# Kernel tuning notes

Measured on AMD Instinct MI355X. Metric: run time of the kernel, lower is better.

The kernel has to match this reference:

```python
import jax, jax.numpy as jnp
import numpy as np

B, S, H, STEPS = 4096, 169, 64, 24  # batch, input seq (window 168 + covariate row), hidden, rollout steps


def _lstm(xseq, Wih, Whh, bih, bhh, h0, c0):
    """PyTorch-style single-layer LSTM. xseq: [B,T,D] -> ([B,T,H], hT, cT). Gate order i,f,g,o."""
    xg = jnp.einsum('btd,gd->btg', xseq, Wih) + (bih + bhh)  # precompute input proj [B,T,4H]

    def step(carry, xg_t):
        h, c = carry
        g = xg_t + h @ Whh.T
        i, f, gg, o = jnp.split(g, 4, axis=-1)
        c = jax.nn.sigmoid(f) * c + jax.nn.sigmoid(i) * jnp.tanh(gg)
        h = jax.nn.sigmoid(o) * jnp.tanh(c)
        return (h, c), h

    (hT, cT), hs = jax.lax.scan(step, (h0, c0), jnp.swapaxes(xg, 0, 1))
    return jnp.swapaxes(hs, 0, 1), hT, cT


def reference(x, Wih1, Whh1, bih1, bhh1, Wih2, Whh2, bih2, bhh2, fc1_w, fc1_b, fc2_w, fc2_b):
    win, d = x[:, :-1, :], x[:, -1, :]  # [B,168,1], [B,1]
    z = jnp.zeros((x.shape[0], H), x.dtype)

    def outer(win, _):
        h1s, h1, c1 = _lstm(win, Wih1, Whh1, bih1, bhh1, z, z)
        h1s = jax.nn.relu(h1s)
        # lstm2 is seeded with lstm1's final (h, c) state, as in the torch code
        h2s, _, _ = _lstm(h1s, Wih2, Whh2, bih2, bhh2, h1, c1)
        feat = jnp.concatenate([jax.nn.relu(h2s[:, -1, :]), d], axis=1)  # [B,65]
        out = (feat @ fc1_w.T + fc1_b) @ fc2_w.T + fc2_b  # [B,1] (no relu between fc1/fc2)
        win = jnp.concatenate([win[:, 1:, :], out[:, :, None]], axis=1)  # slide window
        return win, out[:, 0]

    _, outs = jax.lax.scan(outer, win, None, length=STEPS)  # outs: [24,B]
    return jnp.swapaxes(outs, 0, 1)  # [B,24]


def setup_inputs() -> dict:
    key = jax.random.key(0)
    ks = jax.random.split(key, 14)
    bnd = 1.0 / np.sqrt(H)

    def u(k, shape):
        return jax.random.uniform(k, shape, jnp.float32, -bnd, bnd)

    return {
        'x': jax.random.normal(ks[0], (B, S, 1), jnp.float32),
        'Wih1': u(ks[1], (4 * H, 1)),
        'Whh1': u(ks[2], (4 * H, H)),
        'bih1': u(ks[3], (4 * H,)),
        'bhh1': u(ks[4], (4 * H,)),
        'Wih2': u(ks[5], (4 * H, H)),
        'Whh2': u(ks[6], (4 * H, H)),
        'bih2': u(ks[7], (4 * H,)),
        'bhh2': u(ks[8], (4 * H,)),
        'fc1_w': u(ks[9], (64, 65)),
        'fc1_b': u(ks[10], (64,)),
        'fc2_w': u(ks[11], (1, 64)),
        'fc2_b': u(ks[12], (1,)),
    }
```

## Files before the change

kernel.cpp:

```cpp
#include <hip/hip_runtime.h>
#include <stdint.h>

#define NB 16
#define WIN 168
#define NSTEPS 24
#define NBLK (4096/NB)
#define NT 512

typedef __attribute__((ext_vector_type(8))) short bf16x8;
typedef __attribute__((ext_vector_type(4))) float f32x4;

#if __has_builtin(__builtin_amdgcn_rcpf)
#define RCPF(x) __builtin_amdgcn_rcpf(x)
#else
#define RCPF(x) (1.0f / (x))
#endif
#if __has_builtin(__builtin_amdgcn_exp2f)
#define EXP2F(x) __builtin_amdgcn_exp2f(x)
#else
#define EXP2F(x) __expf((x) * 0.6931471805599453f)
#endif

__device__ __forceinline__ float sigm(float x){
  return RCPF(1.0f + EXP2F(x * -1.4426950408889634f));
}
__device__ __forceinline__ float sigtanh(float a, float b){
  float A = EXP2F(a * -1.4426950408889634f);
  float B = EXP2F(fabsf(b) * -2.8853900817779268f);
  float t = (1.0f - B) * RCPF((1.0f + A) * (1.0f + B));
  uint32_t sb = __builtin_bit_cast(uint32_t, b) & 0x80000000u;
  return __builtin_bit_cast(float, __builtin_bit_cast(uint32_t, t) ^ sb);
}

__device__ __forceinline__ uint32_t bf_rn(float f){
  uint32_t u = __builtin_bit_cast(uint32_t, f);
  return (u + 0x7FFFu + ((u >> 16) & 1u)) >> 16;
}
__device__ __forceinline__ float bf_f(uint32_t s){
  return __builtin_bit_cast(float, s << 16);
}
__device__ __forceinline__ void split_t(float f, uint32_t& hi, uint32_t& lo){
  uint32_t u = __builtin_bit_cast(uint32_t, f);
  hi = u >> 16;
  lo = bf_rn(f - bf_f(hi));
}
__device__ __forceinline__ void split_s(float f, short& hi, short& lo){
  uint32_t h = bf_rn(f);
  hi = (short)h;
  lo = (short)bf_rn(f - bf_f(h));
}
__device__ __forceinline__ f32x4 mfma16(bf16x8 a, bf16x8 b, f32x4 c){
  return __builtin_amdgcn_mfma_f32_16x16x32_bf16(a, b, c, 0, 0, 0);
}

__device__ __forceinline__ void lstm_epi(const f32x4 acc[4], float c[4], float hn[4]){
  #pragma unroll
  for (int r = 0; r < 4; r++){
    float cn = __builtin_fmaf(sigm(acc[1][r]), c[r], sigtanh(acc[0][r], acc[2][r]));
    c[r] = cn;
    hn[r] = sigtanh(acc[3][r], cn);
  }
}

#define FROW 136
#define FBLK 544
#define FB(buf,hl,kt) ((((buf)*2 + (hl))*2 + (kt)) * FBLK)
#define BUF_INTS (2*FBLK)

__global__ __launch_bounds__(NT, 2) void lstm_fused_kernel(
  const float* __restrict__ x,    const float* __restrict__ Wih1, const float* __restrict__ Whh1,
  const float* __restrict__ bih1, const float* __restrict__ bhh1,
  const float* __restrict__ Wih2, const float* __restrict__ Whh2,
  const float* __restrict__ bih2, const float* __restrict__ bhh2,
  const float* __restrict__ fc1w, const float* __restrict__ fc1b,
  const float* __restrict__ fc2w, const float* __restrict__ fc2b,
  float* __restrict__ out, short* __restrict__ hist)
{
  __shared__ __align__(16) short aS[2*2*2*FBLK];
  __shared__ __align__(16) short bS[2*2*2*FBLK];
  __shared__ float cS[64][16];
  __shared__ float win_s[WIN][NB];
  __shared__ float Hlast[NB][68];
  __shared__ float fc1w_s[64*68];
  __shared__ float dval_s[NB];

  const int tid = threadIdx.x;
  const int wv8 = tid >> 6;
  const int wv  = wv8 & 3;
  const bool isA = (wv8 < 4);
  const int ln  = tid & 63;
  const int q   = ln >> 4;
  const int n   = ln & 15;
  const int bg0 = blockIdx.x * NB;
  const int u0  = 16*wv + 4*q;
  const int kt_  = u0 >> 5;
  const int q2_  = (u0 >> 3) & 3;
  const int jj0_ = u0 & 7;
  const int rdo  = q*FROW + n*8;
  const int wro  = q2_*FROW + n*8 + jj0_;
  const int gwo  = kt_*512 + q2_*128 + n*8 + jj0_;
  const int ro   = q*128 + n*8;
  short* __restrict__ hblk = hist + (size_t)blockIdx.x * WIN * 2048;

  for (int i = tid; i < WIN*NB; i += NT){ int t = i >> 4, b = i & 15; win_s[t][b] = x[(bg0 + b)*169 + t]; }
  for (int i = tid; i < 64*65; i += NT){ int j = i / 65, k = i % 65; fc1w_s[j*68 + k] = fc1w[i]; }
  if (tid < NB) dval_s[tid] = x[(bg0 + tid)*169 + 168];

  const float fc1b_r = fc1b[ln];
  const float fc2w_r = fc2w[ln];
  const float fc2b_r = fc2b[0];

  auto fc_head = [&](int s){
    float o2[2];
    #pragma unroll
    for (int bi = 0; bi < 2; bi++){
      const int b = 2*wv8 + bi;
      float a1 = fc1b_r;
      #pragma unroll
      for (int k4 = 0; k4 < 16; k4++){
        const float* wp = &fc1w_s[ln*68 + k4*4];
        const float* hp = &Hlast[b][k4*4];
        a1 += wp[0]*hp[0] + wp[1]*hp[1] + wp[2]*hp[2] + wp[3]*hp[3];
      }
      a1 += dval_s[b] * fc1w_s[ln*68 + 64];
      float v = a1 * fc2w_r;
      #pragma unroll
      for (int off = 32; off > 0; off >>= 1) v += __shfl_xor(v, off);
      o2[bi] = v + fc2b_r;
    }
    if (ln == 0){
      #pragma unroll
      for (int bi = 0; bi < 2; bi++){
        const int b = 2*wv8 + bi;
        out[(bg0 + b)*24 + s] = o2[bi];
        win_s[s % WIN][b] = o2[bi];
      }
    }
  };

  if (isA){
    bf16x8 A1hi[4][2], A1lo[4][2], Ain1[4];
    f32x4 b1c[4];
    #pragma unroll
    for (int e = 0; e < 4; e++){
      const int ja = 64*e + 16*wv + n;
      #pragma unroll
      for (int kt = 0; kt < 2; kt++){
        const float* p = Whh1 + ja*64 + kt*32 + q*8;
        #pragma unroll
        for (int jj = 0; jj < 8; jj++){ short h,l; split_s(p[jj], h, l); A1hi[e][kt][jj] = h; A1lo[e][kt][jj] = l; }
      }
      bf16x8 ain = {0,0,0,0,0,0,0,0};
      if (q == 0){ short wh, wl; split_s(Wih1[ja], wh, wl); ain[0] = wh; ain[1] = wh; ain[2] = wl; }
      Ain1[e] = ain;
      const int jc = 64*e + u0;
      #pragma unroll
      for (int r = 0; r < 4; r++) b1c[e][r] = bih1[jc+r] + bhh1[jc+r];
    }
    float c1[4];

    auto lstm1 = [&](int rb, int wb, int slot, int t, bool first){
      f32x4 acc[4];
      bf16x8 bin = {0,0,0,0,0,0,0,0};
      { float xv = win_s[slot][n]; uint32_t xh, xl; split_t(xv, xh, xl);
        if (q == 0){ bin[0] = (short)xh; bin[1] = (short)xl; bin[2] = (short)xh; } }
      if (first){
        #pragma unroll
        for (int e = 0; e < 4; e++) acc[e] = mfma16(Ain1[e], bin, b1c[e]);
      } else {
        bf16x8 Bh0 = *(const bf16x8*)&aS[FB(rb,0,0)+rdo];
        bf16x8 Bl0 = *(const bf16x8*)&aS[FB(rb,1,0)+rdo];
        bf16x8 Bh1 = *(const bf16x8*)&aS[FB(rb,0,1)+rdo];
        bf16x8 Bl1 = *(const bf16x8*)&aS[FB(rb,1,1)+rdo];
        #pragma unroll
        for (int e = 0; e < 4; e++){
          f32x4 a = b1c[e];
          a = mfma16(A1hi[e][0], Bh0, a);
          a = mfma16(A1hi[e][0], Bl0, a);
          a = mfma16(A1lo[e][0], Bh0, a);
          a = mfma16(A1hi[e][1], Bh1, a);
          a = mfma16(A1hi[e][1], Bl1, a);
          a = mfma16(A1lo[e][1], Bh1, a);
          a = mfma16(Ain1[e], bin, a);
          acc[e] = a;
        }
      }
      float hn[4];
      lstm_epi(acc, c1, hn);
      uint32_t ph[4], pl[4];
      #pragma unroll
      for (int r = 0; r < 4; r++) split_t(hn[r], ph[r], pl[r]);
      *(uint2*)&aS[FB(wb,0,kt_)+wro] = make_uint2(ph[0] | (ph[1]<<16), ph[2] | (ph[3]<<16));
      *(uint2*)&aS[FB(wb,1,kt_)+wro] = make_uint2(pl[0] | (pl[1]<<16), pl[2] | (pl[3]<<16));
      uint32_t sh[4], sl[4];
      #pragma unroll
      for (int r = 0; r < 4; r++){ bool pos = hn[r] > 0.0f; sh[r] = pos ? ph[r] : 0u; sl[r] = pos ? pl[r] : 0u; }
      short* Hp = hblk + (size_t)t * 2048;
      *(uint2*)&Hp[gwo]        = make_uint2(sh[0] | (sh[1]<<16), sh[2] | (sh[3]<<16));
      *(uint2*)&Hp[1024 + gwo] = make_uint2(sl[0] | (sl[1]<<16), sl[2] | (sl[3]<<16));
    };

    #pragma unroll
    for (int r = 0; r < 4; r++) c1[r] = 0.0f;
    for (int t = 0; t < WIN; t++){
      __syncthreads();
      lstm1(t & 1, (t & 1) ^ 1, t, t, t == 0);
    }
    #pragma unroll
    for (int r = 0; r < 4; r++) cS[u0 + r][n] = c1[r];

    for (int sg = 1; sg < NSTEPS; sg++){
      #pragma unroll
      for (int r = 0; r < 4; r++) c1[r] = 0.0f;
      int slot = sg;
      __syncthreads();
      lstm1(0, 1, slot, 0, true);
      slot++;
      for (int t = 1; t < WIN-1; t++){
        __syncthreads();
        lstm1(t & 1, (t & 1) ^ 1, slot, t, false);
        slot++; if (slot == WIN) slot = 0;
      }
      __syncthreads();
      __syncthreads();
      fc_head(sg - 1);
      __syncthreads();
      lstm1(1, 0, slot, WIN-1, false);
      #pragma unroll
      for (int r = 0; r < 4; r++) cS[u0 + r][n] = c1[r];
    }

    for (int i = 0; i < WIN + 1; i++) __syncthreads();
    fc_head(NSTEPS - 1);

  } else {
    bf16x8 A2hi[4][4], A2lo[4][4];
    f32x4 b2c[4];
    #pragma unroll
    for (int e = 0; e < 4; e++){
      const int ja = 64*e + 16*wv + n;
      #pragma unroll
      for (int kt = 0; kt < 4; kt++){
        const float* p = (kt < 2 ? (Wih2 + ja*64 + kt*32) : (Whh2 + ja*64 + (kt-2)*32)) + q*8;
        #pragma unroll
        for (int jj = 0; jj < 8; jj++){ short h,l; split_s(p[jj], h, l); A2hi[e][kt][jj] = h; A2lo[e][kt][jj] = l; }
      }
      const int jc = 64*e + u0;
      #pragma unroll
      for (int r = 0; r < 4; r++) b2c[e][r] = bih2[jc+r] + bhh2[jc+r];
    }
    float c2[4];
    bf16x8 ch0, cl0, ch1, cl1, nh0, nl0, nh1, nl1;

    auto loadc = [&](int t){
      const short* Hp = hblk + (size_t)t * 2048;
      ch0 = *(const bf16x8*)&Hp[ro];
      cl0 = *(const bf16x8*)&Hp[1024 + ro];
      ch1 = *(const bf16x8*)&Hp[512 + ro];
      cl1 = *(const bf16x8*)&Hp[1536 + ro];
    };
    auto loadn = [&](int t){
      const short* Hp = hblk + (size_t)t * 2048;
      nh0 = *(const bf16x8*)&Hp[ro];
      nl0 = *(const bf16x8*)&Hp[1024 + ro];
      nh1 = *(const bf16x8*)&Hp[512 + ro];
      nl1 = *(const bf16x8*)&Hp[1536 + ro];
    };
    auto shift = [&](){ ch0 = nh0; cl0 = nl0; ch1 = nh1; cl1 = nl1; };

    auto lstm2 = [&](const short* Sr, int rb, short* Sw, int wb, bool last){
      bf16x8 L2h0 = *(const bf16x8*)&Sr[FB(rb,0,0)+rdo];
      bf16x8 L2l0 = *(const bf16x8*)&Sr[FB(rb,1,0)+rdo];
      bf16x8 L2h1 = *(const bf16x8*)&Sr[FB(rb,0,1)+rdo];
      bf16x8 L2l1 = *(const bf16x8*)&Sr[FB(rb,1,1)+rdo];
      f32x4 acc[4];
      #pragma unroll
      for (int e = 0; e < 4; e++){
        f32x4 a = b2c[e];
        a = mfma16(A2hi[e][0], ch0, a);
        a = mfma16(A2hi[e][0], cl0, a);
        a = mfma16(A2lo[e][0], ch0, a);
        a = mfma16(A2hi[e][1], ch1, a);
        a = mfma16(A2hi[e][1], cl1, a);
        a = mfma16(A2lo[e][1], ch1, a);
        a = mfma16(A2hi[e][2], L2h0, a);
        a = mfma16(A2hi[e][2], L2l0, a);
        a = mfma16(A2lo[e][2], L2h0, a);
        a = mfma16(A2hi[e][3], L2h1, a);
        a = mfma16(A2hi[e][3], L2l1, a);
        a = mfma16(A2lo[e][3], L2h1, a);
        acc[e] = a;
      }
      float hn[4];
      lstm_epi(acc, c2, hn);
      if (!last){
        uint32_t ph[4], pl[4];
        #pragma unroll
        for (int r = 0; r < 4; r++) split_t(hn[r], ph[r], pl[r]);
        *(uint2*)&Sw[FB(wb,0,kt_)+wro] = make_uint2(ph[0] | (ph[1]<<16), ph[2] | (ph[3]<<16));
        *(uint2*)&Sw[FB(wb,1,kt_)+wro] = make_uint2(pl[0] | (pl[1]<<16), pl[2] | (pl[3]<<16));
      } else {
        #pragma unroll
        for (int r = 0; r < 4; r++) Hlast[n][u0 + r] = fmaxf(hn[r], 0.0f);
      }
    };

    for (int i = 0; i < WIN; i++) __syncthreads();

    for (int sg = 1; sg < NSTEPS; sg++){
      loadc(0);
      loadn(1);
      __syncthreads();
      #pragma unroll
      for (int r = 0; r < 4; r++) c2[r] = cS[u0 + r][n];
      lstm2(aS, 0, bS, 1, false);
      shift();
      for (int t = 1; t < WIN-1; t++){
        loadn(t + 1);
        __syncthreads();
        lstm2(bS, t & 1, bS, (t & 1) ^ 1, false);
        shift();
      }
      __syncthreads();
      lstm2(bS, 1, bS, 0, true);
      __syncthreads();
      fc_head(sg - 1);
      __syncthreads();
    }

    {
      loadc(0);
      loadn(1);
      __syncthreads();
      #pragma unroll
      for (int r = 0; r < 4; r++) c2[r] = cS[u0 + r][n];
      lstm2(aS, 0, bS, 1, false);
      shift();
      for (int t = 1; t < WIN; t++){
        if (t < WIN-1) loadn(t + 1);
        __syncthreads();
        lstm2(bS, t & 1, bS, (t & 1) ^ 1, t == WIN-1);
        shift();
      }
      __syncthreads();
      fc_head(NSTEPS - 1);
    }
  }
}

__global__ __launch_bounds__(256, 1) void lstm_fallback_kernel(
  const float* __restrict__ x,    const float* __restrict__ Wih1, const float* __restrict__ Whh1,
  const float* __restrict__ bih1, const float* __restrict__ bhh1,
  const float* __restrict__ Wih2, const float* __restrict__ Whh2,
  const float* __restrict__ bih2, const float* __restrict__ bhh2,
  const float* __restrict__ fc1w, const float* __restrict__ fc1b,
  const float* __restrict__ fc2w, const float* __restrict__ fc2b,
  float* __restrict__ out)
{
  __shared__ __align__(16) short aS[2*2*2*FBLK];
  __shared__ __align__(16) short r1f[2*2*2*FBLK];
  __shared__ __align__(16) short rlf[2*2*2*FBLK];
  __shared__ float win_s[WIN][NB];
  __shared__ float Hlast[NB][68];
  __shared__ float fc1w_s[64*68];
  __shared__ float dval_s[NB];

  const int tid = threadIdx.x;
  const int wv  = tid >> 6;
  const int ln  = tid & 63;
  const int q   = ln >> 4;
  const int n   = ln & 15;
  const int bg0 = blockIdx.x * NB;
  const int u0  = 16*wv + 4*q;
  const int kt_  = u0 >> 5;
  const int q2_  = (u0 >> 3) & 3;
  const int jj0_ = u0 & 7;
  const int rdo  = q*FROW + n*8;
  const int wro  = q2_*FROW + n*8 + jj0_;

  for (int i = tid; i < WIN*NB; i += 256){ int t = i >> 4, b = i & 15; win_s[t][b] = x[(bg0 + b)*169 + t]; }
  for (int i = tid; i < 64*65; i += 256){ int j = i / 65, k = i % 65; fc1w_s[j*68 + k] = fc1w[i]; }
  if (tid < NB) dval_s[tid] = x[(bg0 + tid)*169 + 168];

  const float fc1b_r = fc1b[ln];
  const float fc2w_r = fc2w[ln];
  const float fc2b_r = fc2b[0];

  bf16x8 A1hi[4][2], A1lo[4][2], Ain1[4];
  bf16x8 A2hi[4][4], A2lo[4][4];
  f32x4 b1c[4], b2c[4];
  #pragma unroll
  for (int e = 0; e < 4; e++){
    const int ja = 64*e + 16*wv + n;
    #pragma unroll
    for (int kt = 0; kt < 2; kt++){
      const float* p = Whh1 + ja*64 + kt*32 + q*8;
      #pragma unroll
      for (int jj = 0; jj < 8; jj++){ short h,l; split_s(p[jj], h, l); A1hi[e][kt][jj] = h; A1lo[e][kt][jj] = l; }
    }
    #pragma unroll
    for (int kt = 0; kt < 4; kt++){
      const float* p = (kt < 2 ? (Wih2 + ja*64 + kt*32) : (Whh2 + ja*64 + (kt-2)*32)) + q*8;
      #pragma unroll
      for (int jj = 0; jj < 8; jj++){ short h,l; split_s(p[jj], h, l); A2hi[e][kt][jj] = h; A2lo[e][kt][jj] = l; }
    }
    bf16x8 ain = {0,0,0,0,0,0,0,0};
    if (q == 0){ short wh, wl; split_s(Wih1[ja], wh, wl); ain[0] = wh; ain[1] = wh; ain[2] = wl; }
    Ain1[e] = ain;
    const int jc = 64*e + u0;
    #pragma unroll
    for (int r = 0; r < 4; r++){
      b1c[e][r] = bih1[jc+r] + bhh1[jc+r];
      b2c[e][r] = bih2[jc+r] + bhh2[jc+r];
    }
  }

  float c1[4], c2[4], c1r[4];

  auto lstm1_step = [&](short* S, float* cst, int rb, int wb, int slot, bool relu_out){
    bf16x8 Bh0 = *(const bf16x8*)&S[FB(rb,0,0)+rdo];
    bf16x8 Bl0 = *(const bf16x8*)&S[FB(rb,1,0)+rdo];
    bf16x8 Bh1 = *(const bf16x8*)&S[FB(rb,0,1)+rdo];
    bf16x8 Bl1 = *(const bf16x8*)&S[FB(rb,1,1)+rdo];
    bf16x8 bin = {0,0,0,0,0,0,0,0};
    { float xv = win_s[slot][n]; uint32_t xh, xl; split_t(xv, xh, xl);
      if (q == 0){ bin[0] = (short)xh; bin[1] = (short)xl; bin[2] = (short)xh; } }
    f32x4 acc[4];
    #pragma unroll
    for (int e = 0; e < 4; e++){
      f32x4 a = b1c[e];
      a = mfma16(A1hi[e][0], Bh0, a);
      a = mfma16(A1hi[e][0], Bl0, a);
      a = mfma16(A1lo[e][0], Bh0, a);
      a = mfma16(A1hi[e][1], Bh1, a);
      a = mfma16(A1hi[e][1], Bl1, a);
      a = mfma16(A1lo[e][1], Bh1, a);
      a = mfma16(Ain1[e], bin, a);
      acc[e] = a;
    }
    float hn[4];
    lstm_epi(acc, cst, hn);
    uint32_t ph[4], pl[4];
    #pragma unroll
    for (int r = 0; r < 4; r++) split_t(hn[r], ph[r], pl[r]);
    *(uint2*)&S[FB(wb,0,kt_)+wro] = make_uint2(ph[0] | (ph[1]<<16), ph[2] | (ph[3]<<16));
    *(uint2*)&S[FB(wb,1,kt_)+wro] = make_uint2(pl[0] | (pl[1]<<16), pl[2] | (pl[3]<<16));
    if (relu_out){
      uint32_t sh[4], sl[4];
      #pragma unroll
      for (int r = 0; r < 4; r++){ bool pos = hn[r] > 0.0f; sh[r] = pos ? ph[r] : 0u; sl[r] = pos ? pl[r] : 0u; }
      *(uint2*)&rlf[FB(rb,0,kt_)+wro] = make_uint2(sh[0] | (sh[1]<<16), sh[2] | (sh[3]<<16));
      *(uint2*)&rlf[FB(rb,1,kt_)+wro] = make_uint2(sl[0] | (sl[1]<<16), sl[2] | (sl[3]<<16));
    }
  };

  auto lstm2_core = [&](bf16x8 L1h0, bf16x8 L1l0, bf16x8 L1h1, bf16x8 L1l1,
                        int rbuf, int wbuf, bool last){
    bf16x8 L2h0 = *(const bf16x8*)&aS[FB(rbuf,0,0)+rdo];
    bf16x8 L2l0 = *(const bf16x8*)&aS[FB(rbuf,1,0)+rdo];
    bf16x8 L2h1 = *(const bf16x8*)&aS[FB(rbuf,0,1)+rdo];
    bf16x8 L2l1 = *(const bf16x8*)&aS[FB(rbuf,1,1)+rdo];
    f32x4 acc[4];
    #pragma unroll
    for (int e = 0; e < 4; e++){
      f32x4 a = b2c[e];
      a = mfma16(A2hi[e][0], L1h0, a);
      a = mfma16(A2hi[e][0], L1l0, a);
      a = mfma16(A2lo[e][0], L1h0, a);
      a = mfma16(A2hi[e][1], L1h1, a);
      a = mfma16(A2hi[e][1], L1l1, a);
      a = mfma16(A2lo[e][1], L1h1, a);
      a = mfma16(A2hi[e][2], L2h0, a);
      a = mfma16(A2hi[e][2], L2l0, a);
      a = mfma16(A2lo[e][2], L2h0, a);
      a = mfma16(A2hi[e][3], L2h1, a);
      a = mfma16(A2hi[e][3], L2l1, a);
      a = mfma16(A2lo[e][3], L2h1, a);
      acc[e] = a;
    }
    float hn[4];
    lstm_epi(acc, c2, hn);
    if (!last){
      uint32_t ph[4], pl[4];
      #pragma unroll
      for (int r = 0; r < 4; r++) split_t(hn[r], ph[r], pl[r]);
      *(uint2*)&aS[FB(wbuf,0,kt_)+wro] = make_uint2(ph[0] | (ph[1]<<16), ph[2] | (ph[3]<<16));
      *(uint2*)&aS[FB(wbuf,1,kt_)+wro] = make_uint2(pl[0] | (pl[1]<<16), pl[2] | (pl[3]<<16));
    } else {
      #pragma unroll
      for (int r = 0; r < 4; r++) Hlast[n][u0 + r] = fmaxf(hn[r], 0.0f);
    }
  };

  for (int s = 0; s < NSTEPS; s++){
    { int* p = (int*)&aS[0];
      for (int i = tid; i < BUF_INTS; i += 256) p[i] = 0; }
    #pragma unroll
    for (int r = 0; r < 4; r++) c1[r] = 0.0f;
    int slot = s;
    for (int t = 0; t < WIN; t++){
      __syncthreads();
      lstm1_step(aS, c1, t & 1, (t & 1) ^ 1, slot, false);
      slot++; if (slot == WIN) slot = 0;
    }
    #pragma unroll
    for (int r = 0; r < 4; r++){ c2[r] = c1[r]; c1r[r] = 0.0f; }
    { int* p = (int*)&r1f[0];
      for (int i = tid; i < BUF_INTS; i += 256) p[i] = 0; }
    slot = s;
    __syncthreads();
    lstm1_step(r1f, c1r, 0, 1, slot, true);
    slot++;
    for (int i = 1; i < WIN; i++){
      __syncthreads();
      const int rb = i & 1, wb = rb ^ 1;
      lstm1_step(r1f, c1r, rb, wb, slot, true);
      bf16x8 L1h0 = *(const bf16x8*)&rlf[FB(wb,0,0)+rdo];
      bf16x8 L1l0 = *(const bf16x8*)&rlf[FB(wb,1,0)+rdo];
      bf16x8 L1h1 = *(const bf16x8*)&rlf[FB(wb,0,1)+rdo];
      bf16x8 L1l1 = *(const bf16x8*)&rlf[FB(wb,1,1)+rdo];
      lstm2_core(L1h0, L1l0, L1h1, L1l1, wb, rb, false);
      slot++; if (slot == WIN) slot = 0;
    }
    __syncthreads();
    {
      const int rb = (WIN - 1) & 1;
      bf16x8 L1h0 = *(const bf16x8*)&rlf[FB(rb,0,0)+rdo];
      bf16x8 L1l0 = *(const bf16x8*)&rlf[FB(rb,1,0)+rdo];
      bf16x8 L1h1 = *(const bf16x8*)&rlf[FB(rb,0,1)+rdo];
      bf16x8 L1l1 = *(const bf16x8*)&rlf[FB(rb,1,1)+rdo];
      lstm2_core(L1h0, L1l0, L1h1, L1l1, rb, 0, true);
    }
    __syncthreads();
    {
      float o4[4];
      #pragma unroll
      for (int bi = 0; bi < 4; bi++){
        const int b = 4*wv + bi;
        float a1 = fc1b_r;
        #pragma unroll
        for (int k4 = 0; k4 < 16; k4++){
          const float* wp = &fc1w_s[ln*68 + k4*4];
          const float* hp = &Hlast[b][k4*4];
          a1 += wp[0]*hp[0] + wp[1]*hp[1] + wp[2]*hp[2] + wp[3]*hp[3];
        }
        a1 += dval_s[b] * fc1w_s[ln*68 + 64];
        float v = a1 * fc2w_r;
        #pragma unroll
        for (int off = 32; off > 0; off >>= 1) v += __shfl_xor(v, off);
        o4[bi] = v + fc2b_r;
      }
      if (ln == 0){
        #pragma unroll
        for (int bi = 0; bi < 4; bi++){
          const int b = 4*wv + bi;
          out[(bg0 + b)*24 + s] = o4[bi];
          win_s[s % WIN][b] = o4[bi];
        }
      }
    }
  }
}

extern "C" void kernel_launch(void* const* d_in, const int* in_sizes, int n_in,
                              void* d_out, int out_size, void* d_ws, size_t ws_size,
                              hipStream_t stream) {
  (void)in_sizes; (void)n_in; (void)out_size;
  const size_t need = (size_t)NBLK * WIN * 2048 * sizeof(short);
  if (ws_size >= need){
    lstm_fused_kernel<<<dim3(NBLK), dim3(NT), 0, stream>>>(
        (const float*)d_in[0], (const float*)d_in[1], (const float*)d_in[2],
        (const float*)d_in[3], (const float*)d_in[4], (const float*)d_in[5],
        (const float*)d_in[6], (const float*)d_in[7], (const float*)d_in[8],
        (const float*)d_in[9], (const float*)d_in[10], (const float*)d_in[11],
        (const float*)d_in[12], (float*)d_out, (short*)d_ws);
  } else {
    lstm_fallback_kernel<<<dim3(NBLK), dim3(256), 0, stream>>>(
        (const float*)d_in[0], (const float*)d_in[1], (const float*)d_in[2],
        (const float*)d_in[3], (const float*)d_in[4], (const float*)d_in[5],
        (const float*)d_in[6], (const float*)d_in[7], (const float*)d_in[8],
        (const float*)d_in[9], (const float*)d_in[10], (const float*)d_in[11],
        (const float*)d_in[12], (float*)d_out);
  }
}
```

Baseline: 5.111 ms.

## Split LSTM1 and LSTM2 into separate producer/consumer blocks with flag sync

The fused 512-thread block, in which the LSTM1 waves and LSTM2 waves lock-step on shared barriers, is replaced by pairs of 256-thread blocks. One block runs LSTM1 and the other runs LSTM2 plus the FC head, and they exchange hidden history, final cell state and outputs through global workspace using atomic progress counters and spin-waits. The aim is to let the two layers run decoupled, so LSTM1 can run up to a window ahead instead of stalling on joint barriers. The cost is global-memory handoff, fences and polling. Correctness depends on all paired blocks being co-resident, and the fallback kernel for small workspaces is removed.

```diff
diff --git a/kernel.cpp b/kernel.cpp
--- a/kernel.cpp
+++ b/kernel.cpp
@@ -4,7 +4,7 @@
 #define NB 16
 #define WIN 168
 #define NSTEPS 24
-#define NBLK (4096/NB)
+#define PAIRS (4096/NB)
 #define NT 512
 
 typedef __attribute__((ext_vector_type(8))) short bf16x8;
@@ -66,6 +66,291 @@
 #define FBLK 544
 #define FB(buf,hl,kt) ((((buf)*2 + (hl))*2 + (kt)) * FBLK)
 #define BUF_INTS (2*FBLK)
+
+#define HIST_SHORTS ((size_t)PAIRS * WIN * 2048)
+#define HIST_BYTES  (HIST_SHORTS * 2)
+#define CFIN_FLOATS ((size_t)PAIRS * 1024)
+#define CFIN_BYTES  (CFIN_FLOATS * 4)
+#define PROG_BYTES  ((size_t)2 * PAIRS * 4)
+
+__global__ __launch_bounds__(256, 2) void lstm_decoupled_kernel(
+  const float* __restrict__ x,    const float* __restrict__ Wih1, const float* __restrict__ Whh1,
+  const float* __restrict__ bih1, const float* __restrict__ bhh1,
+  const float* __restrict__ Wih2, const float* __restrict__ Whh2,
+  const float* __restrict__ bih2, const float* __restrict__ bhh2,
+  const float* __restrict__ fc1w, const float* __restrict__ fc1b,
+  const float* __restrict__ fc2w, const float* __restrict__ fc2b,
+  float* __restrict__ out, short* __restrict__ hist,
+  float* __restrict__ cfin, unsigned* __restrict__ prog)
+{
+  __shared__ __align__(16) short aS[2*2*2*FBLK];
+  __shared__ __align__(16) short bS[2*2*2*FBLK];
+  __shared__ float win_s[WIN][NB];
+  __shared__ float Hlast[NB][68];
+  __shared__ float fc1w_s[64*68];
+  __shared__ float dval_s[NB];
+
+  const int p   = blockIdx.x >> 1;
+  const bool isA = (blockIdx.x & 1) == 0;
+  const int tid = threadIdx.x;
+  const int wv  = tid >> 6;
+  const int ln  = tid & 63;
+  const int q   = ln >> 4;
+  const int n   = ln & 15;
+  const int bg0 = p * NB;
+  const int u0  = 16*wv + 4*q;
+  const int kt_  = u0 >> 5;
+  const int q2_  = (u0 >> 3) & 3;
+  const int jj0_ = u0 & 7;
+  const int rdo  = q*FROW + n*8;
+  const int wro  = q2_*FROW + n*8 + jj0_;
+  const int gwo  = kt_*512 + q2_*128 + n*8 + jj0_;
+  const int ro   = q*128 + n*8;
+  short*    __restrict__ hblk = hist + (size_t)p * WIN * 2048;
+  float*    __restrict__ cfp  = cfin + (size_t)p * 1024;
+  unsigned* Ap = prog + p;
+  unsigned* Bp = prog + PAIRS + p;
+
+  if (isA){
+    for (int i = tid; i < WIN*NB; i += 256){ int t = i >> 4, b = i & 15; win_s[t][b] = x[(bg0 + b)*169 + t]; }
+
+    bf16x8 A1hi[4][2], A1lo[4][2], Ain1[4];
+    f32x4 b1c[4];
+    #pragma unroll
+    for (int e = 0; e < 4; e++){
+      const int ja = 64*e + 16*wv + n;
+      #pragma unroll
+      for (int kt = 0; kt < 2; kt++){
+        const float* pw = Whh1 + ja*64 + kt*32 + q*8;
+        #pragma unroll
+        for (int jj = 0; jj < 8; jj++){ short h,l; split_s(pw[jj], h, l); A1hi[e][kt][jj] = h; A1lo[e][kt][jj] = l; }
+      }
+      bf16x8 ain = {0,0,0,0,0,0,0,0};
+      if (q == 0){ short wh, wl; split_s(Wih1[ja], wh, wl); ain[0] = wh; ain[1] = wh; ain[2] = wl; }
+      Ain1[e] = ain;
+      const int jc = 64*e + u0;
+      #pragma unroll
+      for (int r = 0; r < 4; r++) b1c[e][r] = bih1[jc+r] + bhh1[jc+r];
+    }
+    float c1[4];
+    unsigned bp_cache = 0;
+
+    for (int sg = 0; sg < NSTEPS; sg++){
+      #pragma unroll
+      for (int r = 0; r < 4; r++) c1[r] = 0.0f;
+      int slot = sg;
+      for (int t = 0; t < WIN; t++){
+        const int g = sg*WIN + t;
+        if (tid == 0){
+          const int limit = g - (WIN - 1);
+          if ((int)bp_cache < limit){
+            while ((int)(bp_cache = atomicAdd(Bp, 0u)) < limit) __builtin_amdgcn_s_sleep(8);
+          }
+        }
+        __syncthreads();
+        if (t == WIN-1 && sg > 0){
+          if (tid == 0) __threadfence();
+          __syncthreads();
+          if (tid < NB) win_s[sg-1][tid] = out[(bg0 + tid)*24 + (sg-1)];
+          __syncthreads();
+        }
+        {
+          const int rb = t & 1, wb = rb ^ 1;
+          const bool first = (t == 0);
+          f32x4 acc[4];
+          bf16x8 bin = {0,0,0,0,0,0,0,0};
+          { float xv = win_s[slot][n]; uint32_t xh, xl; split_t(xv, xh, xl);
+            if (q == 0){ bin[0] = (short)xh; bin[1] = (short)xl; bin[2] = (short)xh; } }
+          if (first){
+            #pragma unroll
+            for (int e = 0; e < 4; e++) acc[e] = mfma16(Ain1[e], bin, b1c[e]);
+          } else {
+            bf16x8 Bh0 = *(const bf16x8*)&aS[FB(rb,0,0)+rdo];
+            bf16x8 Bl0 = *(const bf16x8*)&aS[FB(rb,1,0)+rdo];
+            bf16x8 Bh1 = *(const bf16x8*)&aS[FB(rb,0,1)+rdo];
+            bf16x8 Bl1 = *(const bf16x8*)&aS[FB(rb,1,1)+rdo];
+            #pragma unroll
+            for (int e = 0; e < 4; e++){
+              f32x4 a = b1c[e];
+              a = mfma16(A1hi[e][0], Bh0, a);
+              a = mfma16(A1hi[e][0], Bl0, a);
+              a = mfma16(A1lo[e][0], Bh0, a);
+              a = mfma16(A1hi[e][1], Bh1, a);
+              a = mfma16(A1hi[e][1], Bl1, a);
+              a = mfma16(A1lo[e][1], Bh1, a);
+              a = mfma16(Ain1[e], bin, a);
+              acc[e] = a;
+            }
+          }
+          float hn[4];
+          lstm_epi(acc, c1, hn);
+          uint32_t ph[4], pl[4];
+          #pragma unroll
+          for (int r = 0; r < 4; r++) split_t(hn[r], ph[r], pl[r]);
+          *(uint2*)&aS[FB(wb,0,kt_)+wro] = make_uint2(ph[0] | (ph[1]<<16), ph[2] | (ph[3]<<16));
+          *(uint2*)&aS[FB(wb,1,kt_)+wro] = make_uint2(pl[0] | (pl[1]<<16), pl[2] | (pl[3]<<16));
+          short* Hp = hblk + (size_t)t * 2048;
+          if (t < WIN-1){
+            uint32_t sh[4], sl[4];
+            #pragma unroll
+            for (int r = 0; r < 4; r++){ bool pos = hn[r] > 0.0f; sh[r] = pos ? ph[r] : 0u; sl[r] = pos ? pl[r] : 0u; }
+            *(uint2*)&Hp[gwo]        = make_uint2(sh[0] | (sh[1]<<16), sh[2] | (sh[3]<<16));
+            *(uint2*)&Hp[1024 + gwo] = make_uint2(sl[0] | (sl[1]<<16), sl[2] | (sl[3]<<16));
+          } else {
+            *(uint2*)&Hp[gwo]        = make_uint2(ph[0] | (ph[1]<<16), ph[2] | (ph[3]<<16));
+            *(uint2*)&Hp[1024 + gwo] = make_uint2(pl[0] | (pl[1]<<16), pl[2] | (pl[3]<<16));
+          }
+        }
+        slot++; if (slot == WIN) slot = 0;
+      }
+      #pragma unroll
+      for (int r = 0; r < 4; r++) cfp[(u0 + r)*16 + n] = c1[r];
+      __syncthreads();
+      if (tid == 0){ __threadfence(); atomicExch(Ap, (unsigned)((sg+1)*WIN)); }
+    }
+
+  } else {
+    for (int i = tid; i < 64*65; i += 256){ int j = i / 65, k = i % 65; fc1w_s[j*68 + k] = fc1w[i]; }
+    if (tid < NB) dval_s[tid] = x[(bg0 + tid)*169 + 168];
+
+    bf16x8 A2hi[4][4], A2lo[4][4];
+    f32x4 b2c[4];
+    #pragma unroll
+    for (int e = 0; e < 4; e++){
+      const int ja = 64*e + 16*wv + n;
+      #pragma unroll
+      for (int kt = 0; kt < 4; kt++){
+        const float* pw = (kt < 2 ? (Wih2 + ja*64 + kt*32) : (Whh2 + ja*64 + (kt-2)*32)) + q*8;
+        #pragma unroll
+        for (int jj = 0; jj < 8; jj++){ short h,l; split_s(pw[jj], h, l); A2hi[e][kt][jj] = h; A2lo[e][kt][jj] = l; }
+      }
+      const int jc = 64*e + u0;
+      #pragma unroll
+      for (int r = 0; r < 4; r++) b2c[e][r] = bih2[jc+r] + bhh2[jc+r];
+    }
+    const float fc1b_r = fc1b[ln];
+    const float fc2w_r = fc2w[ln];
+    const float fc2b_r = fc2b[0];
+    float c2[4];
+    bf16x8 ch0, cl0, ch1, cl1, nh0, nl0, nh1, nl1;
+
+    auto loadn = [&](int t){
+      const short* Hp = hblk + (size_t)t * 2048;
+      nh0 = *(const bf16x8*)&Hp[ro];
+      nl0 = *(const bf16x8*)&Hp[1024 + ro];
+      nh1 = *(const bf16x8*)&Hp[512 + ro];
+      nl1 = *(const bf16x8*)&Hp[1536 + ro];
+    };
+    auto relufix = [&](bf16x8& h, bf16x8& l){
+      #pragma unroll
+      for (int j = 0; j < 8; j++){
+        bool neg = (h[j] & (short)0x8000) != 0;
+        h[j] = neg ? (short)0 : h[j];
+        l[j] = neg ? (short)0 : l[j];
+      }
+    };
+
+    for (int sb = 0; sb < NSTEPS; sb++){
+      if (tid == 0){
+        const unsigned need_a = (unsigned)((sb+1)*WIN);
+        while (atomicAdd(Ap, 0u) < need_a) __builtin_amdgcn_s_sleep(8);
+        __threadfence();
+      }
+      __syncthreads();
+      #pragma unroll
+      for (int r = 0; r < 4; r++) c2[r] = cfp[(u0 + r)*16 + n];
+      {
+        const short* Hp = hblk + (size_t)(WIN-1) * 2048;
+        bf16x8 s0 = *(const bf16x8*)&Hp[ro];
+        bf16x8 s1 = *(const bf16x8*)&Hp[1024 + ro];
+        bf16x8 s2 = *(const bf16x8*)&Hp[512 + ro];
+        bf16x8 s3 = *(const bf16x8*)&Hp[1536 + ro];
+        if (wv == 0){
+          *(bf16x8*)&bS[FB(0,0,0)+rdo] = s0;
+          *(bf16x8*)&bS[FB(0,1,0)+rdo] = s1;
+          *(bf16x8*)&bS[FB(0,0,1)+rdo] = s2;
+          *(bf16x8*)&bS[FB(0,1,1)+rdo] = s3;
+        }
+      }
+      loadn(0); ch0 = nh0; cl0 = nl0; ch1 = nh1; cl1 = nl1;
+      __syncthreads();
+
+      for (int t = 0; t < WIN; t++){
+        if (t < WIN-1) loadn(t + 1);
+        if (t){
+          __syncthreads();
+          if (tid == 0 && (t & 15) == 0) atomicExch(Bp, (unsigned)(sb*WIN + t));
+        }
+        const bool last = (t == WIN-1);
+        if (last){ relufix(ch0, cl0); relufix(ch1, cl1); }
+        {
+          const int rb = t & 1, wb = rb ^ 1;
+          bf16x8 L2h0 = *(const bf16x8*)&bS[FB(rb,0,0)+rdo];
+          bf16x8 L2l0 = *(const bf16x8*)&bS[FB(rb,1,0)+rdo];
+          bf16x8 L2h1 = *(const bf16x8*)&bS[FB(rb,0,1)+rdo];
+          bf16x8 L2l1 = *(const bf16x8*)&bS[FB(rb,1,1)+rdo];
+          f32x4 acc[4];
+          #pragma unroll
+          for (int e = 0; e < 4; e++){
+            f32x4 a = b2c[e];
+            a = mfma16(A2hi[e][0], ch0, a);
+            a = mfma16(A2hi[e][0], cl0, a);
+            a = mfma16(A2lo[e][0], ch0, a);
+            a = mfma16(A2hi[e][1], ch1, a);
+            a = mfma16(A2hi[e][1], cl1, a);
+            a = mfma16(A2lo[e][1], ch1, a);
+            a = mfma16(A2hi[e][2], L2h0, a);
+            a = mfma16(A2hi[e][2], L2l0, a);
+            a = mfma16(A2lo[e][2], L2h0, a);
+            a = mfma16(A2hi[e][3], L2h1, a);
+            a = mfma16(A2hi[e][3], L2l1, a);
+            a = mfma16(A2lo[e][3], L2h1, a);
+            acc[e] = a;
+          }
+          float hn[4];
+          lstm_epi(acc, c2, hn);
+          if (!last){
+            uint32_t ph[4], pl[4];
+            #pragma unroll
+            for (int r = 0; r < 4; r++) split_t(hn[r], ph[r], pl[r]);
+            *(uint2*)&bS[FB(wb,0,kt_)+wro] = make_uint2(ph[0] | (ph[1]<<16), ph[2] | (ph[3]<<16));
+            *(uint2*)&bS[FB(wb,1,kt_)+wro] = make_uint2(pl[0] | (pl[1]<<16), pl[2] | (pl[3]<<16));
+          } else {
+            #pragma unroll
+            for (int r = 0; r < 4; r++) Hlast[n][u0 + r] = fmaxf(hn[r], 0.0f);
+          }
+        }
+        ch0 = nh0; cl0 = nl0; ch1 = nh1; cl1 = nl1;
+      }
+      __syncthreads();
+      {
+        float o4[4];
+        #pragma unroll
+        for (int bi = 0; bi < 4; bi++){
+          const int b = 4*wv + bi;
+          float a1 = fc1b_r;
+          #pragma unroll
+          for (int k4 = 0; k4 < 16; k4++){
+            const float* wp = &fc1w_s[ln*68 + k4*4];
+            const float* hp = &Hlast[b][k4*4];
+            a1 += wp[0]*hp[0] + wp[1]*hp[1] + wp[2]*hp[2] + wp[3]*hp[3];
+          }
+          a1 += dval_s[b] * fc1w_s[ln*68 + 64];
+          float v = a1 * fc2w_r;
+          #pragma unroll
+          for (int off = 32; off > 0; off >>= 1) v += __shfl_xor(v, off);
+          o4[bi] = v + fc2b_r;
+        }
+        if (ln == 0){
+          #pragma unroll
+          for (int bi = 0; bi < 4; bi++) out[(bg0 + 4*wv + bi)*24 + sb] = o4[bi];
+        }
+      }
+      __syncthreads();
+      if (tid == 0){ __threadfence(); atomicExch(Bp, (unsigned)((sb+1)*WIN)); }
+    }
+  }
+}
 
 __global__ __launch_bounds__(NT, 2) void lstm_fused_kernel(
   const float* __restrict__ x,    const float* __restrict__ Wih1, const float* __restrict__ Whh1,
@@ -146,9 +431,9 @@
       const int ja = 64*e + 16*wv + n;
       #pragma unroll
       for (int kt = 0; kt < 2; kt++){
-        const float* p = Whh1 + ja*64 + kt*32 + q*8;
-        #pragma unroll
-        for (int jj = 0; jj < 8; jj++){ short h,l; split_s(p[jj], h, l); A1hi[e][kt][jj] = h; A1lo[e][kt][jj] = l; }
+        const float* pw = Whh1 + ja*64 + kt*32 + q*8;
+        #pragma unroll
+        for (int jj = 0; jj < 8; jj++){ short h,l; split_s(pw[jj], h, l); A1hi[e][kt][jj] = h; A1lo[e][kt][jj] = l; }
       }
       bf16x8 ain = {0,0,0,0,0,0,0,0};
       if (q == 0){ short wh, wl; split_s(Wih1[ja], wh, wl); ain[0] = wh; ain[1] = wh; ain[2] = wl; }
@@ -229,7 +514,6 @@
       #pragma unroll
       for (int r = 0; r < 4; r++) cS[u0 + r][n] = c1[r];
     }
-
     for (int i = 0; i < WIN + 1; i++) __syncthreads();
     fc_head(NSTEPS - 1);
 
@@ -241,9 +525,9 @@
       const int ja = 64*e + 16*wv + n;
       #pragma unroll
       for (int kt = 0; kt < 4; kt++){
-        const float* p = (kt < 2 ? (Wih2 + ja*64 + kt*32) : (Whh2 + ja*64 + (kt-2)*32)) + q*8;
-        #pragma unroll
-        for (int jj = 0; jj < 8; jj++){ short h,l; split_s(p[jj], h, l); A2hi[e][kt][jj] = h; A2lo[e][kt][jj] = l; }
+        const float* pw = (kt < 2 ? (Wih2 + ja*64 + kt*32) : (Whh2 + ja*64 + (kt-2)*32)) + q*8;
+        #pragma unroll
+        for (int jj = 0; jj < 8; jj++){ short h,l; split_s(pw[jj], h, l); A2hi[e][kt][jj] = h; A2lo[e][kt][jj] = l; }
       }
       const int jc = 64*e + u0;
       #pragma unroll
@@ -327,7 +611,6 @@
       fc_head(sg - 1);
       __syncthreads();
     }
-
     {
       loadc(0);
       loadn(1);
@@ -348,238 +631,30 @@
   }
 }
 
-__global__ __launch_bounds__(256, 1) void lstm_fallback_kernel(
-  const float* __restrict__ x,    const float* __restrict__ Wih1, const float* __restrict__ Whh1,
-  const float* __restrict__ bih1, const float* __restrict__ bhh1,
-  const float* __restrict__ Wih2, const float* __restrict__ Whh2,
-  const float* __restrict__ bih2, const float* __restrict__ bhh2,
-  const float* __restrict__ fc1w, const float* __restrict__ fc1b,
-  const float* __restrict__ fc2w, const float* __restrict__ fc2b,
-  float* __restrict__ out)
-{
-  __shared__ __align__(16) short aS[2*2*2*FBLK];
-  __shared__ __align__(16) short r1f[2*2*2*FBLK];
-  __shared__ __align__(16) short rlf[2*2*2*FBLK];
-  __shared__ float win_s[WIN][NB];
-  __shared__ float Hlast[NB][68];
-  __shared__ float fc1w_s[64*68];
-  __shared__ float dval_s[NB];
-
-  const int tid = threadIdx.x;
-  const int wv  = tid >> 6;
-  const int ln  = tid & 63;
-  const int q   = ln >> 4;
-  const int n   = ln & 15;
-  const int bg0 = blockIdx.x * NB;
-  const int u0  = 16*wv + 4*q;
-  const int kt_  = u0 >> 5;
-  const int q2_  = (u0 >> 3) & 3;
-  const int jj0_ = u0 & 7;
-  const int rdo  = q*FROW + n*8;
-  const int wro  = q2_*FROW + n*8 + jj0_;
-
-  for (int i = tid; i < WIN*NB; i += 256){ int t = i >> 4, b = i & 15; win_s[t][b] = x[(bg0 + b)*169 + t]; }
-  for (int i = tid; i < 64*65; i += 256){ int j = i / 65, k = i % 65; fc1w_s[j*68 + k] = fc1w[i]; }
-  if (tid < NB) dval_s[tid] = x[(bg0 + tid)*169 + 168];
-
-  const float fc1b_r = fc1b[ln];
-  const float fc2w_r = fc2w[ln];
-  const float fc2b_r = fc2b[0];
-
-  bf16x8 A1hi[4][2], A1lo[4][2], Ain1[4];
-  bf16x8 A2hi[4][4], A2lo[4][4];
-  f32x4 b1c[4], b2c[4];
-  #pragma unroll
-  for (int e = 0; e < 4; e++){
-    const int ja = 64*e + 16*wv + n;
-    #pragma unroll
-    for (int kt = 0; kt < 2; kt++){
-      const float* p = Whh1 + ja*64 + kt*32 + q*8;
-      #pragma unroll
-      for (int jj = 0; jj < 8; jj++){ short h,l; split_s(p[jj], h, l); A1hi[e][kt][jj] = h; A1lo[e][kt][jj] = l; }
-    }
-    #pragma unroll
-    for (int kt = 0; kt < 4; kt++){
-      const float* p = (kt < 2 ? (Wih2 + ja*64 + kt*32) : (Whh2 + ja*64 + (kt-2)*32)) + q*8;
-      #pragma unroll
-      for (int jj = 0; jj < 8; jj++){ short h,l; split_s(p[jj], h, l); A2hi[e][kt][jj] = h; A2lo[e][kt][jj] = l; }
-    }
-    bf16x8 ain = {0,0,0,0,0,0,0,0};
-    if (q == 0){ short wh, wl; split_s(Wih1[ja], wh, wl); ain[0] = wh; ain[1] = wh; ain[2] = wl; }
-    Ain1[e] = ain;
-    const int jc = 64*e + u0;
-    #pragma unroll
-    for (int r = 0; r < 4; r++){
-      b1c[e][r] = bih1[jc+r] + bhh1[jc+r];
-      b2c[e][r] = bih2[jc+r] + bhh2[jc+r];
-    }
-  }
-
-  float c1[4], c2[4], c1r[4];
-
-  auto lstm1_step = [&](short* S, float* cst, int rb, int wb, int slot, bool relu_out){
-    bf16x8 Bh0 = *(const bf16x8*)&S[FB(rb,0,0)+rdo];
-    bf16x8 Bl0 = *(const bf16x8*)&S[FB(rb,1,0)+rdo];
-    bf16x8 Bh1 = *(const bf16x8*)&S[FB(rb,0,1)+rdo];
-    bf16x8 Bl1 = *(const bf16x8*)&S[FB(rb,1,1)+rdo];
-    bf16x8 bin = {0,0,0,0,0,0,0,0};
-    { float xv = win_s[slot][n]; uint32_t xh, xl; split_t(xv, xh, xl);
-      if (q == 0){ bin[0] = (short)xh; bin[1] = (short)xl; bin[2] = (short)xh; } }
-    f32x4 acc[4];
-    #pragma unroll
-    for (int e = 0; e < 4; e++){
-      f32x4 a = b1c[e];
-      a = mfma16(A1hi[e][0], Bh0, a);
-      a = mfma16(A1hi[e][0], Bl0, a);
-      a = mfma16(A1lo[e][0], Bh0, a);
-      a = mfma16(A1hi[e][1], Bh1, a);
-      a = mfma16(A1hi[e][1], Bl1, a);
-      a = mfma16(A1lo[e][1], Bh1, a);
-      a = mfma16(Ain1[e], bin, a);
-      acc[e] = a;
-    }
-    float hn[4];
-    lstm_epi(acc, cst, hn);
-    uint32_t ph[4], pl[4];
-    #pragma unroll
-    for (int r = 0; r < 4; r++) split_t(hn[r], ph[r], pl[r]);
-    *(uint2*)&S[FB(wb,0,kt_)+wro] = make_uint2(ph[0] | (ph[1]<<16), ph[2] | (ph[3]<<16));
-    *(uint2*)&S[FB(wb,1,kt_)+wro] = make_uint2(pl[0] | (pl[1]<<16), pl[2] | (pl[3]<<16));
-    if (relu_out){
-      uint32_t sh[4], sl[4];
-      #pragma unroll
-      for (int r = 0; r < 4; r++){ bool pos = hn[r] > 0.0f; sh[r] = pos ? ph[r] : 0u; sl[r] = pos ? pl[r] : 0u; }
-      *(uint2*)&rlf[FB(rb,0,kt_)+wro] = make_uint2(sh[0] | (sh[1]<<16), sh[2] | (sh[3]<<16));
-      *(uint2*)&rlf[FB(rb,1,kt_)+wro] = make_uint2(sl[0] | (sl[1]<<16), sl[2] | (sl[3]<<16));
-    }
-  };
-
-  auto lstm2_core = [&](bf16x8 L1h0, bf16x8 L1l0, bf16x8 L1h1, bf16x8 L1l1,
-                        int rbuf, int wbuf, bool last){
-    bf16x8 L2h0 = *(const bf16x8*)&aS[FB(rbuf,0,0)+rdo];
-    bf16x8 L2l0 = *(const bf16x8*)&aS[FB(rbuf,1,0)+rdo];
-    bf16x8 L2h1 = *(const bf16x8*)&aS[FB(rbuf,0,1)+rdo];
-    bf16x8 L2l1 = *(const bf16x8*)&aS[FB(rbuf,1,1)+rdo];
-    f32x4 acc[4];
-    #pragma unroll
-    for (int e = 0; e < 4; e++){
-      f32x4 a = b2c[e];
-      a = mfma16(A2hi[e][0], L1h0, a);
-      a = mfma16(A2hi[e][0], L1l0, a);
-      a = mfma16(A2lo[e][0], L1h0, a);
-      a = mfma16(A2hi[e][1], L1h1, a);
-      a = mfma16(A2hi[e][1], L1l1, a);
-      a = mfma16(A2lo[e][1], L1h1, a);
-      a = mfma16(A2hi[e][2], L2h0, a);
-      a = mfma16(A2hi[e][2], L2l0, a);
-      a = mfma16(A2lo[e][2], L2h0, a);
-      a = mfma16(A2hi[e][3], L2h1, a);
-      a = mfma16(A2hi[e][3], L2l1, a);
-      a = mfma16(A2lo[e][3], L2h1, a);
-      acc[e] = a;
-    }
-    float hn[4];
-    lstm_epi(acc, c2, hn);
-    if (!last){
-      uint32_t ph[4], pl[4];
-      #pragma unroll
-      for (int r = 0; r < 4; r++) split_t(hn[r], ph[r], pl[r]);
-      *(uint2*)&aS[FB(wbuf,0,kt_)+wro] = make_uint2(ph[0] | (ph[1]<<16), ph[2] | (ph[3]<<16));
-      *(uint2*)&aS[FB(wbuf,1,kt_)+wro] = make_uint2(pl[0] | (pl[1]<<16), pl[2] | (pl[3]<<16));
-    } else {
-      #pragma unroll
-      for (int r = 0; r < 4; r++) Hlast[n][u0 + r] = fmaxf(hn[r], 0.0f);
-    }
-  };
-
-  for (int s = 0; s < NSTEPS; s++){
-    { int* p = (int*)&aS[0];
-      for (int i = tid; i < BUF_INTS; i += 256) p[i] = 0; }
-    #pragma unroll
-    for (int r = 0; r < 4; r++) c1[r] = 0.0f;
-    int slot = s;
-    for (int t = 0; t < WIN; t++){
-      __syncthreads();
-      lstm1_step(aS, c1, t & 1, (t & 1) ^ 1, slot, false);
-      slot++; if (slot == WIN) slot = 0;
-    }
-    #pragma unroll
-    for (int r = 0; r < 4; r++){ c2[r] = c1[r]; c1r[r] = 0.0f; }
-    { int* p = (int*)&r1f[0];
-      for (int i = tid; i < BUF_INTS; i += 256) p[i] = 0; }
-    slot = s;
-    __syncthreads();
-    lstm1_step(r1f, c1r, 0, 1, slot, true);
-    slot++;
-    for (int i = 1; i < WIN; i++){
-      __syncthreads();
-      const int rb = i & 1, wb = rb ^ 1;
-      lstm1_step(r1f, c1r, rb, wb, slot, true);
-      bf16x8 L1h0 = *(const bf16x8*)&rlf[FB(wb,0,0)+rdo];
-      bf16x8 L1l0 = *(const bf16x8*)&rlf[FB(wb,1,0)+rdo];
-      bf16x8 L1h1 = *(const bf16x8*)&rlf[FB(wb,0,1)+rdo];
-      bf16x8 L1l1 = *(const bf16x8*)&rlf[FB(wb,1,1)+rdo];
-      lstm2_core(L1h0, L1l0, L1h1, L1l1, wb, rb, false);
-      slot++; if (slot == WIN) slot = 0;
-    }
-    __syncthreads();
-    {
-      const int rb = (WIN - 1) & 1;
-      bf16x8 L1h0 = *(const bf16x8*)&rlf[FB(rb,0,0)+rdo];
-      bf16x8 L1l0 = *(const bf16x8*)&rlf[FB(rb,1,0)+rdo];
-      bf16x8 L1h1 = *(const bf16x8*)&rlf[FB(rb,0,1)+rdo];
-      bf16x8 L1l1 = *(const bf16x8*)&rlf[FB(rb,1,1)+rdo];
-      lstm2_core(L1h0, L1l0, L1h1, L1l1, rb, 0, true);
-    }
-    __syncthreads();
-    {
-      float o4[4];
-      #pragma unroll
-      for (int bi = 0; bi < 4; bi++){
-        const int b = 4*wv + bi;
-        float a1 = fc1b_r;
-        #pragma unroll
-        for (int k4 = 0; k4 < 16; k4++){
-          const float* wp = &fc1w_s[ln*68 + k4*4];
-          const float* hp = &Hlast[b][k4*4];
-          a1 += wp[0]*hp[0] + wp[1]*hp[1] + wp[2]*hp[2] + wp[3]*hp[3];
-        }
-        a1 += dval_s[b] * fc1w_s[ln*68 + 64];
-        float v = a1 * fc2w_r;
-        #pragma unroll
-        for (int off = 32; off > 0; off >>= 1) v += __shfl_xor(v, off);
-        o4[bi] = v + fc2b_r;
-      }
-      if (ln == 0){
-        #pragma unroll
-        for (int bi = 0; bi < 4; bi++){
-          const int b = 4*wv + bi;
-          out[(bg0 + b)*24 + s] = o4[bi];
-          win_s[s % WIN][b] = o4[bi];
-        }
-      }
-    }
-  }
-}
-
 extern "C" void kernel_launch(void* const* d_in, const int* in_sizes, int n_in,
                               void* d_out, int out_size, void* d_ws, size_t ws_size,
                               hipStream_t stream) {
   (void)in_sizes; (void)n_in; (void)out_size;
-  const size_t need = (size_t)NBLK * WIN * 2048 * sizeof(short);
-  if (ws_size >= need){
-    lstm_fused_kernel<<<dim3(NBLK), dim3(NT), 0, stream>>>(
+  const size_t need_old = HIST_BYTES;
+  const size_t need_new = HIST_BYTES + CFIN_BYTES + PROG_BYTES;
+  if (ws_size >= need_new){
+    char* ws = (char*)d_ws;
+    short*    hist = (short*)ws;
+    float*    cfin = (float*)(ws + HIST_BYTES);
+    unsigned* prog = (unsigned*)(ws + HIST_BYTES + CFIN_BYTES);
+    hipMemsetAsync((void*)prog, 0, PROG_BYTES, stream);
+    lstm_decoupled_kernel<<<dim3(2*PAIRS), dim3(256), 0, stream>>>(
+        (const float*)d_in[0], (const float*)d_in[1], (const float*)d_in[2],
+        (const float*)d_in[3], (const float*)d_in[4], (const float*)d_in[5],
+        (const float*)d_in[6], (const float*)d_in[7], (const float*)d_in[8],
+        (const float*)d_in[9], (const float*)d_in[10], (const float*)d_in[11],
+        (const float*)d_in[12], (float*)d_out, hist, cfin, prog);
+  } else if (ws_size >= need_old){
+    lstm_fused_kernel<<<dim3(PAIRS), dim3(NT), 0, stream>>>(
         (const float*)d_in[0], (const float*)d_in[1], (const float*)d_in[2],
         (const float*)d_in[3], (const float*)d_in[4], (const float*)d_in[5],
         (const float*)d_in[6], (const float*)d_in[7], (const float*)d_in[8],
         (const float*)d_in[9], (const float*)d_in[10], (const float*)d_in[11],
         (const float*)d_in[12], (float*)d_out, (short*)d_ws);
-  } else {
-    lstm_fallback_kernel<<<dim3(NBLK), dim3(256), 0, stream>>>(
-        (const float*)d_in[0], (const float*)d_in[1], (const float*)d_in[2],
-        (const float*)d_in[3], (const float*)d_in[4], (const float*)d_in[5],
-        (const float*)d_in[6], (const float*)d_in[7], (const float*)d_in[8],
-        (const float*)d_in[9], (const float*)d_in[10], (const float*)d_in[11],
-        (const float*)d_in[12], (float*)d_out);
   }
 }
```

After: 6.162 ms. +20.6%, slower.
